# Kernel optimization log

Measured on AMD Instinct MI355X. Metric: run time of the kernel, lower is better.

The kernel has to match this reference:

```python
import jax, jax.numpy as jnp
import numpy as np

EPS = 1e-8

def _matrix_sqrt(cov):
    # e @ diag(max(w,EPS))**0.5 @ e.T
    w, e = jnp.linalg.eigh(cov)
    w = jnp.maximum(w, EPS)
    return (e * jnp.sqrt(w)[None, :]) @ e.T

def _matrix_sqrt_neg(cov):
    # cov jittered on diagonal, then e @ diag(1/max(w,EPS))**0.5 @ e.T
    D = cov.shape[-1]
    cov = cov * (jnp.ones_like(cov) + jnp.eye(D, dtype=cov.dtype) * 0.001)
    w, e = jnp.linalg.eigh(cov)
    w = jnp.maximum(w, EPS)
    return (e * (1.0 / jnp.sqrt(w))[None, :]) @ e.T

def _match_axis(xc, R, mu, counter):
    # xc: (C, M, D) per-channel rows; R: (C, D, D) accumulated second moment; mu: (C, D)
    mu_test = xc.mean(1, keepdims=True)                      # (C,1,D)
    h = xc - mu_test                                         # centered test features
    cov_train = R / counter - mu[:, :, None] * mu[:, None, :]  # (C,D,D)
    sqrt_train = jax.vmap(_matrix_sqrt)(cov_train)           # (C,D,D)
    M = h.shape[1]
    cov_test = jnp.einsum('cmd,cme->cde', h, h) / M          # (C,D,D)
    neg_sqrt_test = jax.vmap(_matrix_sqrt_neg)(cov_test)     # (C,D,D)
    T = jnp.einsum('cde,cef->cdf', neg_sqrt_test, sqrt_train)  # whiten-then-recolor map
    return jnp.einsum('cmd,cdf->cmf', h, T) + mu[:, None, :]

def reference(x, cov_H, mu_H, cov_W, mu_W, counter):
    N, H, W, C = x.shape
    cnt = jnp.asarray(counter, dtype=x.dtype)
    # H-axis matching: rows of length H, per channel
    xh = x.transpose(3, 0, 2, 1).reshape(C, N * W, H)
    xh = _match_axis(xh, cov_H, mu_H, cnt)
    # W-axis matching: rows of length W, per channel
    xw = xh.reshape(C, N, W, H).transpose(0, 1, 3, 2).reshape(C, N * H, W)
    xw = _match_axis(xw, cov_W, mu_W, cnt)
    return xw.reshape(C, N, H, W).transpose(1, 2, 3, 0)

def setup_inputs() -> dict:
    key = jax.random.key(0)
    k1, k2, k3, k4, k5 = jax.random.split(key, 5)
    N, H, W, C = 64, 56, 56, 256
    counter = 716800  # accumulated sample count (N*W per acc batch)
    x = jax.random.normal(k1, (N, H, W, C), dtype=jnp.float32)
    mu_H = 0.1 * jax.random.normal(k2, (C, H), dtype=jnp.float32)
    mu_W = 0.1 * jax.random.normal(k3, (C, W), dtype=jnp.float32)
    # Build accumulated second moments so R/counter - outer(mu) is PSD
    BH = jax.random.normal(k4, (C, H, H), dtype=jnp.float32)
    SH = jnp.einsum('cij,ckj->cik', BH, BH) / H + 0.1 * jnp.eye(H, dtype=jnp.float32)
    cov_H = (SH + mu_H[:, :, None] * mu_H[:, None, :]) * counter
    BW = jax.random.normal(k5, (C, W, W), dtype=jnp.float32)
    SW = jnp.einsum('cij,ckj->cik', BW, BW) / W + 0.1 * jnp.eye(W, dtype=jnp.float32)
    cov_W = (SW + mu_W[:, :, None] * mu_W[:, None, :]) * counter
    return {"x": x, "cov_H": cov_H, "mu_H": mu_H, "cov_W": cov_W, "mu_W": mu_W, "counter": counter}
```

## Files before the change

kernel.cpp:

```cpp
#include <hip/hip_runtime.h>

#define C_ 256
#define D_ 56
#define N_ 64
#define M_ 3584
#define DD_ 3136
#define PL_ 200704
#define PL4_ 50176
#define NS_ITERS 16

typedef __attribute__((ext_vector_type(8))) short v8s;
typedef __attribute__((ext_vector_type(8))) _Float16 v8h;
typedef __attribute__((ext_vector_type(4))) _Float16 v4h;
typedef __attribute__((ext_vector_type(4))) float v4f;

__device__ __forceinline__ unsigned short f2bf(float f) {
  union { float f; unsigned u; } x; x.f = f;
  unsigned r = x.u + 0x7FFFu + ((x.u >> 16) & 1u);
  return (unsigned short)(r >> 16);
}
__device__ __forceinline__ float bf2f(unsigned short h) {
  union { unsigned u; float f; } x; x.u = ((unsigned)h) << 16;
  return x.f;
}

__global__ __launch_bounds__(256) void k_tin(const float* __restrict__ x, float* __restrict__ A) {
  int b = blockIdx.x;
  int cchunk = b & 3, g = b >> 2;
  int c0 = cchunk * 64;
  int m0 = g * 4;
  int n = m0 / 56, w0 = m0 % 56;
  __shared__ float t[4][56][65];
  int tid = threadIdx.x;
  const float4* x4 = (const float4*)x;
  #pragma unroll
  for (int it = 0; it < 14; ++it) {
    int i = tid + 256*it;
    int mloc = i / 896, r = i % 896;
    int h = r >> 4, cg = r & 15;
    float4 v = x4[((size_t)n*3136 + (size_t)h*56 + (w0+mloc))*64 + (c0>>2) + cg];
    *(float4*)&t[mloc][h][4*cg] = v;
  }
  __syncthreads();
  float4* A4 = (float4*)A;
  #pragma unroll
  for (int it = 0; it < 14; ++it) {
    int j = tid + 256*it;
    int q = j / 14, hg = j % 14;
    int cc = q >> 2, mloc = q & 3;
    float4 o;
    o.x = t[mloc][4*hg+0][cc];
    o.y = t[mloc][4*hg+1][cc];
    o.z = t[mloc][4*hg+2][cc];
    o.w = t[mloc][4*hg+3][cc];
    A4[(size_t)(c0+cc)*PL4_ + (size_t)(m0+mloc)*14 + hg] = o;
  }
}

__device__ __forceinline__ void mm_split_h(const _Float16 (*Ah)[72], const _Float16 (*Al)[72],
                                           const _Float16 (*Bh)[72], const _Float16 (*Bl)[72],
                                           int w, int lr, int lq, v4f (&acc)[4]) {
  v8h ah[2], al[2], bh[4][2], bl[4][2];
  #pragma unroll
  for (int s = 0; s < 2; ++s) {
    int kb = 32*s + 8*lq;
    ah[s] = *(const v8h*)&Ah[16*w + lr][kb];
    al[s] = *(const v8h*)&Al[16*w + lr][kb];
    #pragma unroll
    for (int jt = 0; jt < 4; ++jt) {
      bh[jt][s] = *(const v8h*)&Bh[16*jt + lr][kb];
      bl[jt][s] = *(const v8h*)&Bl[16*jt + lr][kb];
    }
  }
  #pragma unroll
  for (int jt = 0; jt < 4; ++jt) {
    #pragma unroll
    for (int s = 0; s < 2; ++s) {
      acc[jt] = __builtin_amdgcn_mfma_f32_16x16x32_f16(ah[s], bh[jt][s], acc[jt], 0, 0, 0);
      acc[jt] = __builtin_amdgcn_mfma_f32_16x16x32_f16(ah[s], bl[jt][s], acc[jt], 0, 0, 0);
      acc[jt] = __builtin_amdgcn_mfma_f32_16x16x32_f16(al[s], bh[jt][s], acc[jt], 0, 0, 0);
    }
  }
}

__device__ __forceinline__ void store_split_h(_Float16 (*H)[72], _Float16 (*L)[72],
                                              int w, int lr, int lq, const v4f (&val)[4]) {
  #pragma unroll
  for (int jt = 0; jt < 4; ++jt) {
    #pragma unroll
    for (int e = 0; e < 4; ++e) {
      int i = 16*w + 4*lq + e, j = 16*jt + lr;
      float v = val[jt][e];
      _Float16 h = (_Float16)v;
      H[i][j] = h;
      L[i][j] = (_Float16)(v - (float)h);
    }
  }
}

__global__ __launch_bounds__(256) void k_stats(const float* __restrict__ in,
                                               float* __restrict__ muPart,
                                               float* __restrict__ covPart) {
  int b = blockIdx.x;
  int c = b >> 3, s = b & 7;
  const float* p = in + (size_t)c*PL_ + (size_t)(s*448)*56;
  __shared__ __align__(16) char lds[18432];
  unsigned short (*At)[72]  = (unsigned short(*)[72])lds;
  unsigned short (*Alt)[72] = (unsigned short(*)[72])(lds + 9216);
  float (*Qbuf)[66] = (float(*)[66])lds;
  float (*red2)[60] = (float(*)[60])lds;
  int tid = threadIdx.x;
  int cg = tid % 14, rg = tid / 14;
  bool act = tid < 224;
  float4 colsum = make_float4(0.f, 0.f, 0.f, 0.f);

  int l = tid & 63, w = tid >> 6;
  int lr = l & 15, lq = l >> 4;
  v4f zero4 = {0.f, 0.f, 0.f, 0.f};
  v4f accP[4], accQ[4];
  #pragma unroll
  for (int j = 0; j < 4; ++j) { accP[j] = zero4; accQ[j] = zero4; }

  for (int ch = 0; ch < 7; ++ch) {
    __syncthreads();
    const float4* p4 = (const float4*)(p + ch*64*56);
    if (act) {
      int c4 = cg * 4;
      #pragma unroll
      for (int u = 0; u < 4; ++u) {
        int m = u*16 + rg;
        float4 v = p4[m*14 + cg];
        colsum.x += v.x; colsum.y += v.y; colsum.z += v.z; colsum.w += v.w;
        unsigned short h;
        h = f2bf(v.x); At[c4+0][m] = h; Alt[c4+0][m] = f2bf(v.x - bf2f(h));
        h = f2bf(v.y); At[c4+1][m] = h; Alt[c4+1][m] = f2bf(v.y - bf2f(h));
        h = f2bf(v.z); At[c4+2][m] = h; Alt[c4+2][m] = f2bf(v.z - bf2f(h));
        h = f2bf(v.w); At[c4+3][m] = h; Alt[c4+3][m] = f2bf(v.w - bf2f(h));
      }
    }
    __syncthreads();
    #pragma unroll
    for (int s2 = 0; s2 < 2; ++s2) {
      int kb = 32*s2 + 8*lq;
      v8s a = *(const v8s*)&At[16*w + lr][kb];
      #pragma unroll
      for (int j = 0; j < 4; ++j) {
        v8s bh = *(const v8s*)&At[16*j + lr][kb];
        v8s bl = *(const v8s*)&Alt[16*j + lr][kb];
        accP[j] = __builtin_amdgcn_mfma_f32_16x16x32_bf16(a, bh, accP[j], 0, 0, 0);
        accQ[j] = __builtin_amdgcn_mfma_f32_16x16x32_bf16(a, bl, accQ[j], 0, 0, 0);
      }
    }
  }

  __syncthreads();
  if (act) *(float4*)&red2[rg][cg*4] = colsum;
  __syncthreads();
  if (tid < 64) {
    float m = 0.f;
    if (tid < 56) {
      #pragma unroll
      for (int r = 0; r < 16; ++r) m += red2[r][tid];
    }
    muPart[((size_t)s*C_ + c)*64 + tid] = m;
  }
  __syncthreads();

  #pragma unroll
  for (int j = 0; j < 4; ++j) {
    #pragma unroll
    for (int e = 0; e < 4; ++e) {
      int r = 16*w + 4*lq + e, cc = 16*j + lr;
      Qbuf[r][cc] = accQ[j][e];
    }
  }
  __syncthreads();
  float* op = covPart + ((size_t)s*C_ + c)*DD_;
  #pragma unroll
  for (int j = 0; j < 4; ++j) {
    #pragma unroll
    for (int e = 0; e < 4; ++e) {
      int r = 16*w + 4*lq + e, cc = 16*j + lr;
      if (r < 56 && cc < 56) op[r*56 + cc] = accP[j][e] + accQ[j][e] + Qbuf[cc][r];
    }
  }
}

__global__ __launch_bounds__(256) void k_mured(const float* __restrict__ muPart, float* __restrict__ muT) {
  int idx = blockIdx.x*256 + threadIdx.x;
  if (idx >= C_*64) return;
  int c = idx >> 6, lane = idx & 63;
  float s = 0.f;
  for (int p = 0; p < 8; ++p) s += muPart[((size_t)p*C_ + c)*64 + lane];
  muT[idx] = s * (1.0f/M_);
}

__global__ __launch_bounds__(256) void k_finalize(const float* __restrict__ covPart, const float* __restrict__ muT,
                                                  const float* __restrict__ covIn, const float* __restrict__ muTrn,
                                                  const int* __restrict__ counter,
                                                  float* __restrict__ covTest, float* __restrict__ covTr) {
  int idx = blockIdx.x*256 + threadIdx.x;
  const int total = C_*DD_;
  if (idx < total) {
    int c = idx / DD_, r2 = idx % DD_, i = r2/56, j = r2%56;
    float ssum = 0.f;
    for (int s = 0; s < 8; ++s) ssum += covPart[((size_t)s*C_ + c)*DD_ + r2];
    float v = ssum*(1.0f/M_) - muT[c*64+i]*muT[c*64+j];
    if (i == j) v *= 1.001f;
    covTest[idx] = v;
  } else if (idx < 2*total) {
    int k = idx - total;
    int c = k / DD_, r2 = k % DD_, i = r2/56, j = r2%56;
    float cnt = (float)counter[0];
    covTr[k] = covIn[k]/cnt - muTrn[c*56+i]*muTrn[c*56+j];
  }
}

__global__ __launch_bounds__(256) void k_ns(const float* __restrict__ covTr, const float* __restrict__ covTest,
                                            float* __restrict__ Sout, float* __restrict__ Zout) {
  __shared__ __align__(16) _Float16 mats[6][64][72];
  __shared__ float red[4];
  int tid = threadIdx.x;
  int which = blockIdx.x & 1, c = blockIdx.x >> 1;
  const float4* Ain4 = (const float4*)((which ? covTest : covTr) + (size_t)c * DD_);

  typedef _Float16 (*mat_t)[72];
  mat_t Yh = mats[0], Yl = mats[1], Zh = mats[2], Zl = mats[3], Th = mats[4], Tl = mats[5];

  float ss = 0.f;
  for (int i4 = tid; i4 < 784; i4 += 256) {
    float4 v = Ain4[i4];
    ss += v.x*v.x + v.y*v.y + v.z*v.z + v.w*v.w;
  }
  { unsigned* z = (unsigned*)mats; for (int i = tid; i < 13824; i += 256) z[i] = 0u; }
  #pragma unroll
  for (int off = 32; off > 0; off >>= 1) ss += __shfl_down(ss, off, 64);
  if ((tid & 63) == 0) red[tid >> 6] = ss;
  __syncthreads();
  float s = sqrtf(red[0] + red[1] + red[2] + red[3]);
  float inv = 1.f / s;

  for (int i4 = tid; i4 < 784; i4 += 256) {
    float4 v = Ain4[i4];
    int r = i4 / 14, cgx = (i4 % 14) * 4;
    float f0 = v.x*inv, f1 = v.y*inv, f2 = v.z*inv, f3 = v.w*inv;
    v4h hh, ll;
    hh.x = (_Float16)f0; ll.x = (_Float16)(f0 - (float)hh.x);
    hh.y = (_Float16)f1; ll.y = (_Float16)(f1 - (float)hh.y);
    hh.z = (_Float16)f2; ll.z = (_Float16)(f2 - (float)hh.z);
    hh.w = (_Float16)f3; ll.w = (_Float16)(f3 - (float)hh.w);
    *(v4h*)&Yh[r][cgx] = hh;
    *(v4h*)&Yl[r][cgx] = ll;
  }
  if (tid < 56) Zh[tid][tid] = (_Float16)1.0f;
  __syncthreads();

  int lane = tid & 63, w = tid >> 6, lr = lane & 15, lq = lane >> 4;
  v4f zero4 = {0.f, 0.f, 0.f, 0.f};
  float rs = sqrtf(s);
  float fac = which ? (1.f/rs) : rs;
  float* outp = (which ? Zout : Sout) + (size_t)c*DD_;

  for (int it = 0; it < NS_ITERS; ++it) {
    v4f accW[4] = {zero4, zero4, zero4, zero4};
    mm_split_h(Zh, Zl, Yh, Yl, w, lr, lq, accW);
    v4f Tv[4];
    #pragma unroll
    for (int jt = 0; jt < 4; ++jt) {
      #pragma unroll
      for (int e = 0; e < 4; ++e) {
        float dv = (16*w + 4*lq + e == 16*jt + lr) ? 1.5f : 0.f;
        Tv[jt][e] = dv - 0.5f*accW[jt][e];
      }
    }
    store_split_h(Th, Tl, w, lr, lq, Tv);
    __syncthreads();
    if (it == NS_ITERS - 1) {
      v4f accF[4] = {zero4, zero4, zero4, zero4};
      if (which == 0) mm_split_h(Yh, Yl, Th, Tl, w, lr, lq, accF);
      else            mm_split_h(Th, Tl, Zh, Zl, w, lr, lq, accF);
      #pragma unroll
      for (int jt = 0; jt < 4; ++jt) {
        #pragma unroll
        for (int e = 0; e < 4; ++e) {
          int i = 16*w + 4*lq + e, j = 16*jt + lr;
          if (i < 56 && j < 56) outp[i*56 + j] = accF[jt][e] * fac;
        }
      }
    } else {
      v4f accY[4] = {zero4, zero4, zero4, zero4};
      v4f accZ[4] = {zero4, zero4, zero4, zero4};
      mm_split_h(Yh, Yl, Th, Tl, w, lr, lq, accY);
      mm_split_h(Th, Tl, Zh, Zl, w, lr, lq, accZ);
      __syncthreads();
      store_split_h(Yh, Yl, w, lr, lq, accY);
      store_split_h(Zh, Zl, w, lr, lq, accZ);
      __syncthreads();
    }
  }
}

__global__ __launch_bounds__(256) void k_tmap(const float* __restrict__ Zi, const float* __restrict__ Sm,
                                              float* __restrict__ Tm) {
  __shared__ __align__(16) _Float16 mats[4][64][72];
  int c = blockIdx.x, tid = threadIdx.x;
  typedef _Float16 (*mat_t)[72];
  mat_t Ah = mats[0], Al = mats[1], Bh = mats[2], Bl = mats[3];
  { unsigned* z = (unsigned*)mats; for (int i = tid; i < 9216; i += 256) z[i] = 0u; }
  __syncthreads();
  const float4* Z4 = (const float4*)(Zi + (size_t)c*DD_);
  const float4* S4 = (const float4*)(Sm + (size_t)c*DD_);
  for (int i4 = tid; i4 < 784; i4 += 256) {
    int r = i4 / 14, cgx = (i4 % 14) * 4;
    float4 v = Z4[i4];
    v4h hh, ll;
    hh.x = (_Float16)v.x; ll.x = (_Float16)(v.x - (float)hh.x);
    hh.y = (_Float16)v.y; ll.y = (_Float16)(v.y - (float)hh.y);
    hh.z = (_Float16)v.z; ll.z = (_Float16)(v.z - (float)hh.z);
    hh.w = (_Float16)v.w; ll.w = (_Float16)(v.w - (float)hh.w);
    *(v4h*)&Ah[r][cgx] = hh;
    *(v4h*)&Al[r][cgx] = ll;
    v = S4[i4];
    hh.x = (_Float16)v.x; ll.x = (_Float16)(v.x - (float)hh.x);
    hh.y = (_Float16)v.y; ll.y = (_Float16)(v.y - (float)hh.y);
    hh.z = (_Float16)v.z; ll.z = (_Float16)(v.z - (float)hh.z);
    hh.w = (_Float16)v.w; ll.w = (_Float16)(v.w - (float)hh.w);
    *(v4h*)&Bh[r][cgx] = hh;
    *(v4h*)&Bl[r][cgx] = ll;
  }
  __syncthreads();
  int lane = tid & 63, w = tid >> 6, lr = lane & 15, lq = lane >> 4;
  v4f zero4 = {0.f, 0.f, 0.f, 0.f};
  v4f acc[4] = {zero4, zero4, zero4, zero4};
  mm_split_h(Ah, Al, Bh, Bl, w, lr, lq, acc);
  float* op = Tm + (size_t)c*DD_;
  #pragma unroll
  for (int jt = 0; jt < 4; ++jt) {
    #pragma unroll
    for (int e = 0; e < 4; ++e) {
      int i = 16*w + 4*lq + e, j = 16*jt + lr;
      if (i < 56 && j < 56) op[i*56 + j] = acc[jt][e];
    }
  }
}

__global__ __launch_bounds__(256) void k_apply(const float* __restrict__ in, const float* __restrict__ muT,
                                               const float* __restrict__ Tmp, const float* __restrict__ muTrain,
                                               float* __restrict__ out, int stage) {
  int b = blockIdx.x;
  int c = b >> 6, n = b & 63;
  __shared__ __align__(16) char lds[18432];
  _Float16 (*Abf)[72] = (_Float16(*)[72])lds;
  _Float16 (*Tt)[72]  = (_Float16(*)[72])(lds + 9216);
  float (*Y)[67] = (float(*)[67])lds;
  __shared__ float smu[64], smt[64];
  int tid = threadIdx.x;
  if (tid < 64) {
    smu[tid] = muT[c*64 + tid];
    smt[tid] = (tid < 56) ? muTrain[c*56 + tid] : 0.f;
  }
  if (tid < 128) {
    int row = tid & 63;
    _Float16 (*Mz)[72] = (tid < 64) ? Abf : Tt;
    *(float4*)&Mz[row][56] = make_float4(0.f, 0.f, 0.f, 0.f);
  }
  __syncthreads();
  const float4* p4 = (const float4*)(in + (size_t)c*PL_ + (size_t)n*3136);
  const float4* t4 = (const float4*)(Tmp + (size_t)c*DD_);
  for (int i = tid; i < 784; i += 256) {
    float4 v = p4[i];
    int row = i / 14, cgx = (i % 14) * 4;
    v4h pk;
    pk.x = (_Float16)(v.x - smu[cgx+0]);
    pk.y = (_Float16)(v.y - smu[cgx+1]);
    pk.z = (_Float16)(v.z - smu[cgx+2]);
    pk.w = (_Float16)(v.w - smu[cgx+3]);
    *(v4h*)&Abf[row][cgx] = pk;
    float4 t = t4[i];
    Tt[cgx+0][row] = (_Float16)t.x;
    Tt[cgx+1][row] = (_Float16)t.y;
    Tt[cgx+2][row] = (_Float16)t.z;
    Tt[cgx+3][row] = (_Float16)t.w;
  }
  __syncthreads();
  int l = tid & 63, w = tid >> 6;
  int lr = l & 15, lq = l >> 4;
  v4f zero4 = {0.f, 0.f, 0.f, 0.f};
  v4f acc[4];
  #pragma unroll
  for (int j = 0; j < 4; ++j) acc[j] = zero4;
  #pragma unroll
  for (int s = 0; s < 2; ++s) {
    int kb = 32*s + 8*lq;
    v8h a = *(const v8h*)&Abf[16*w + lr][kb];
    #pragma unroll
    for (int j = 0; j < 4; ++j) {
      v8h bb = *(const v8h*)&Tt[16*j + lr][kb];
      acc[j] = __builtin_amdgcn_mfma_f32_16x16x32_f16(a, bb, acc[j], 0, 0, 0);
    }
  }
  __syncthreads();
  #pragma unroll
  for (int j = 0; j < 4; ++j) {
    #pragma unroll
    for (int e = 0; e < 4; ++e) {
      int r = 16*w + 4*lq + e, cc = 16*j + lr;
      Y[r][cc] = acc[j][e] + smt[cc];
    }
  }
  __syncthreads();
  float4* op4 = (float4*)(out + (size_t)c*PL_ + (size_t)n*3136);
  if (stage == 1) {
    for (int i4 = tid; i4 < 784; i4 += 256) {
      int h = i4 / 14, w4 = (i4 % 14) * 4;
      float4 o;
      o.x = Y[w4+0][h]; o.y = Y[w4+1][h]; o.z = Y[w4+2][h]; o.w = Y[w4+3][h];
      op4[i4] = o;
    }
  } else {
    for (int i4 = tid; i4 < 784; i4 += 256) {
      int h = i4 / 14, w4 = (i4 % 14) * 4;
      float4 o;
      o.x = Y[h][w4+0]; o.y = Y[h][w4+1]; o.z = Y[h][w4+2]; o.w = Y[h][w4+3];
      op4[i4] = o;
    }
  }
}

__global__ __launch_bounds__(256) void k_tout(const float* __restrict__ A2, float* __restrict__ out) {
  int b = blockIdx.x;
  int cchunk = b & 3, g = b >> 2;
  int c0 = cchunk * 64;
  int nh0 = g * 4;
  __shared__ float t[4][56][65];
  int tid = threadIdx.x;
  const float4* A4 = (const float4*)A2;
  #pragma unroll
  for (int it = 0; it < 14; ++it) {
    int j = tid + 256*it;
    int q = j / 14, wg = j % 14;
    int cc = q >> 2, mloc = q & 3;
    float4 v = A4[(size_t)(c0+cc)*PL4_ + (size_t)(nh0+mloc)*14 + wg];
    t[mloc][4*wg+0][cc] = v.x;
    t[mloc][4*wg+1][cc] = v.y;
    t[mloc][4*wg+2][cc] = v.z;
    t[mloc][4*wg+3][cc] = v.w;
  }
  __syncthreads();
  float4* o4 = (float4*)out;
  #pragma unroll
  for (int it = 0; it < 14; ++it) {
    int i = tid + 256*it;
    int mloc = i / 896, r = i % 896;
    int w = r >> 4, cg = r & 15;
    float4 o;
    o.x = t[mloc][w][4*cg+0];
    o.y = t[mloc][w][4*cg+1];
    o.z = t[mloc][w][4*cg+2];
    o.w = t[mloc][w][4*cg+3];
    o4[((size_t)(nh0+mloc)*56 + w)*64 + (c0>>2) + cg] = o;
  }
}

extern "C" void kernel_launch(void* const* d_in, const int* in_sizes, int n_in,
                              void* d_out, int out_size, void* d_ws, size_t ws_size,
                              hipStream_t stream) {
  (void)in_sizes; (void)n_in; (void)out_size;
  const float* x    = (const float*)d_in[0];
  const float* covH = (const float*)d_in[1];
  const float* muH  = (const float*)d_in[2];
  const float* covW = (const float*)d_in[3];
  const float* muW  = (const float*)d_in[4];
  const int*   cnt  = (const int*)d_in[5];
  float* out = (float*)d_out;

  char* ws = (char*)d_ws;
  size_t off = 0;
  auto alloc = [&](size_t nfloats) {
    float* p = (float*)(ws + off);
    off += ((nfloats*sizeof(float) + 255) / 256) * 256;
    return p;
  };
  float* A       = alloc((size_t)C_ * PL_);
  float* covPart = alloc((size_t)8 * C_ * DD_);
  float* muPart  = alloc((size_t)8 * C_ * 64);
  float* covTest = alloc((size_t)C_ * DD_);
  float* covTr   = alloc((size_t)C_ * DD_);
  float* Sm      = alloc((size_t)C_ * DD_);
  float* Zim     = alloc((size_t)C_ * DD_);
  float* Tm      = alloc((size_t)C_ * DD_);
  float* muT     = alloc((size_t)C_ * 64);
  if (off > ws_size) return;

  dim3 blk(256);
  const int finGrid = (2*C_*DD_ + 255)/256;

  k_tin<<<dim3(4 * (M_/4)), blk, 0, stream>>>(x, A);

  k_stats   <<<dim3(2048),  blk, 0, stream>>>(A, muPart, covPart);
  k_mured   <<<dim3(64),    blk, 0, stream>>>(muPart, muT);
  k_finalize<<<dim3(finGrid), blk, 0, stream>>>(covPart, muT, covH, muH, cnt, covTest, covTr);
  k_ns      <<<dim3(512),   blk, 0, stream>>>(covTr, covTest, Sm, Zim);
  k_tmap    <<<dim3(256),   blk, 0, stream>>>(Zim, Sm, Tm);
  k_apply   <<<dim3(16384), blk, 0, stream>>>(A, muT, Tm, muH, out, 1);

  k_stats   <<<dim3(2048),  blk, 0, stream>>>(out, muPart, covPart);
  k_mured   <<<dim3(64),    blk, 0, stream>>>(muPart, muT);
  k_finalize<<<dim3(finGrid), blk, 0, stream>>>(covPart, muT, covW, muW, cnt, covTest, covTr);
  k_ns      <<<dim3(512),   blk, 0, stream>>>(covTr, covTest, Sm, Zim);
  k_tmap    <<<dim3(256),   blk, 0, stream>>>(Zim, Sm, Tm);
  k_apply   <<<dim3(16384), blk, 0, stream>>>(out, muT, Tm, muW, A, 2);

  k_tout<<<dim3(4 * (M_/4)), blk, 0, stream>>>(A, out);
}
```

Measured before the change: 579.5 us.

## Store intermediate activation planes in fp16 instead of fp32

The channel-major intermediate buffers written by the input transpose and by each apply stage, and read by the stats, apply and output transpose kernels, become half precision instead of fp32. This halves the global memory traffic of these bandwidth-bound passes, and the load/store loops are rewritten around 8-wide fp16 vectors. The cost is precision: inputs are rounded to fp16 before the covariance statistics are computed. The bf16 hi/lo split used in the statistics therefore no longer recovers full fp32 accuracy, which may loosen agreement with the fp32 reference.

Measured after the change: 500.0 us. 1.16x faster.

```diff
diff --git a/kernel.cpp b/kernel.cpp
--- a/kernel.cpp
+++ b/kernel.cpp
@@ -6,7 +6,6 @@
 #define M_ 3584
 #define DD_ 3136
 #define PL_ 200704
-#define PL4_ 50176
 #define NS_ITERS 16
 
 typedef __attribute__((ext_vector_type(8))) short v8s;
@@ -24,13 +23,13 @@
   return x.f;
 }
 
-__global__ __launch_bounds__(256) void k_tin(const float* __restrict__ x, float* __restrict__ A) {
+__global__ __launch_bounds__(256) void k_tin(const float* __restrict__ x, _Float16* __restrict__ A) {
   int b = blockIdx.x;
   int cchunk = b & 3, g = b >> 2;
   int c0 = cchunk * 64;
   int m0 = g * 4;
   int n = m0 / 56, w0 = m0 % 56;
-  __shared__ float t[4][56][65];
+  __shared__ _Float16 t[4][56][66];
   int tid = threadIdx.x;
   const float4* x4 = (const float4*)x;
   #pragma unroll
@@ -39,21 +38,21 @@
     int mloc = i / 896, r = i % 896;
     int h = r >> 4, cg = r & 15;
     float4 v = x4[((size_t)n*3136 + (size_t)h*56 + (w0+mloc))*64 + (c0>>2) + cg];
-    *(float4*)&t[mloc][h][4*cg] = v;
-  }
-  __syncthreads();
-  float4* A4 = (float4*)A;
-  #pragma unroll
-  for (int it = 0; it < 14; ++it) {
+    t[mloc][h][4*cg+0] = (_Float16)v.x;
+    t[mloc][h][4*cg+1] = (_Float16)v.y;
+    t[mloc][h][4*cg+2] = (_Float16)v.z;
+    t[mloc][h][4*cg+3] = (_Float16)v.w;
+  }
+  __syncthreads();
+  #pragma unroll
+  for (int it = 0; it < 7; ++it) {
     int j = tid + 256*it;
-    int q = j / 14, hg = j % 14;
+    int q = j / 7, hg = j % 7;
     int cc = q >> 2, mloc = q & 3;
-    float4 o;
-    o.x = t[mloc][4*hg+0][cc];
-    o.y = t[mloc][4*hg+1][cc];
-    o.z = t[mloc][4*hg+2][cc];
-    o.w = t[mloc][4*hg+3][cc];
-    A4[(size_t)(c0+cc)*PL4_ + (size_t)(m0+mloc)*14 + hg] = o;
+    v8h o;
+    #pragma unroll
+    for (int k = 0; k < 8; ++k) o[k] = t[mloc][hg*8+k][cc];
+    *(v8h*)&A[(size_t)(c0+cc)*PL_ + (size_t)(m0+mloc)*56 + hg*8] = o;
   }
 }
 
@@ -98,21 +97,21 @@
   }
 }
 
-__global__ __launch_bounds__(256) void k_stats(const float* __restrict__ in,
+__global__ __launch_bounds__(256) void k_stats(const _Float16* __restrict__ in,
                                                float* __restrict__ muPart,
                                                float* __restrict__ covPart) {
   int b = blockIdx.x;
   int c = b >> 3, s = b & 7;
-  const float* p = in + (size_t)c*PL_ + (size_t)(s*448)*56;
+  const _Float16* p = in + (size_t)c*PL_ + (size_t)(s*448)*56;
   __shared__ __align__(16) char lds[18432];
   unsigned short (*At)[72]  = (unsigned short(*)[72])lds;
   unsigned short (*Alt)[72] = (unsigned short(*)[72])(lds + 9216);
   float (*Qbuf)[66] = (float(*)[66])lds;
   float (*red2)[60] = (float(*)[60])lds;
   int tid = threadIdx.x;
-  int cg = tid % 14, rg = tid / 14;
+  int cg = tid % 7, rg = tid / 7;
   bool act = tid < 224;
-  float4 colsum = make_float4(0.f, 0.f, 0.f, 0.f);
+  float cs[8] = {0.f,0.f,0.f,0.f,0.f,0.f,0.f,0.f};
 
   int l = tid & 63, w = tid >> 6;
   int lr = l & 15, lq = l >> 4;
@@ -123,19 +122,19 @@
 
   for (int ch = 0; ch < 7; ++ch) {
     __syncthreads();
-    const float4* p4 = (const float4*)(p + ch*64*56);
     if (act) {
-      int c4 = cg * 4;
-      #pragma unroll
-      for (int u = 0; u < 4; ++u) {
-        int m = u*16 + rg;
-        float4 v = p4[m*14 + cg];
-        colsum.x += v.x; colsum.y += v.y; colsum.z += v.z; colsum.w += v.w;
-        unsigned short h;
-        h = f2bf(v.x); At[c4+0][m] = h; Alt[c4+0][m] = f2bf(v.x - bf2f(h));
-        h = f2bf(v.y); At[c4+1][m] = h; Alt[c4+1][m] = f2bf(v.y - bf2f(h));
-        h = f2bf(v.z); At[c4+2][m] = h; Alt[c4+2][m] = f2bf(v.z - bf2f(h));
-        h = f2bf(v.w); At[c4+3][m] = h; Alt[c4+3][m] = f2bf(v.w - bf2f(h));
+      #pragma unroll
+      for (int u = 0; u < 2; ++u) {
+        int m = rg + 32*u;
+        v8h v = *(const v8h*)&p[(size_t)(ch*64 + m)*56 + cg*8];
+        #pragma unroll
+        for (int k = 0; k < 8; ++k) {
+          float f = (float)v[k];
+          cs[k] += f;
+          unsigned short h = f2bf(f);
+          At[cg*8+k][m] = h;
+          Alt[cg*8+k][m] = f2bf(f - bf2f(h));
+        }
       }
     }
     __syncthreads();
@@ -154,13 +153,16 @@
   }
 
   __syncthreads();
-  if (act) *(float4*)&red2[rg][cg*4] = colsum;
+  if (act) {
+    #pragma unroll
+    for (int k = 0; k < 8; ++k) red2[rg][cg*8+k] = cs[k];
+  }
   __syncthreads();
   if (tid < 64) {
     float m = 0.f;
     if (tid < 56) {
       #pragma unroll
-      for (int r = 0; r < 16; ++r) m += red2[r][tid];
+      for (int r = 0; r < 32; ++r) m += red2[r][tid];
     }
     muPart[((size_t)s*C_ + c)*64 + tid] = m;
   }
@@ -344,9 +346,9 @@
   }
 }
 
-__global__ __launch_bounds__(256) void k_apply(const float* __restrict__ in, const float* __restrict__ muT,
+__global__ __launch_bounds__(256) void k_apply(const _Float16* __restrict__ in, const float* __restrict__ muT,
                                                const float* __restrict__ Tmp, const float* __restrict__ muTrain,
-                                               float* __restrict__ out, int stage) {
+                                               _Float16* __restrict__ out, int stage) {
   int b = blockIdx.x;
   int c = b >> 6, n = b & 63;
   __shared__ __align__(16) char lds[18432];
@@ -365,18 +367,19 @@
     *(float4*)&Mz[row][56] = make_float4(0.f, 0.f, 0.f, 0.f);
   }
   __syncthreads();
-  const float4* p4 = (const float4*)(in + (size_t)c*PL_ + (size_t)n*3136);
+  const v8h* p8 = (const v8h*)(in + (size_t)c*PL_ + (size_t)n*3136);
   const float4* t4 = (const float4*)(Tmp + (size_t)c*DD_);
+  for (int i = tid; i < 392; i += 256) {
+    int row = i / 7, cg = i % 7;
+    v8h v = p8[row*7 + cg];
+    v8h pk;
+    #pragma unroll
+    for (int k = 0; k < 8; ++k) pk[k] = (_Float16)((float)v[k] - smu[cg*8+k]);
+    *(v8h*)&Abf[row][cg*8] = pk;
+  }
   for (int i = tid; i < 784; i += 256) {
-    float4 v = p4[i];
+    float4 t = t4[i];
     int row = i / 14, cgx = (i % 14) * 4;
-    v4h pk;
-    pk.x = (_Float16)(v.x - smu[cgx+0]);
-    pk.y = (_Float16)(v.y - smu[cgx+1]);
-    pk.z = (_Float16)(v.z - smu[cgx+2]);
-    pk.w = (_Float16)(v.w - smu[cgx+3]);
-    *(v4h*)&Abf[row][cgx] = pk;
-    float4 t = t4[i];
     Tt[cgx+0][row] = (_Float16)t.x;
     Tt[cgx+1][row] = (_Float16)t.y;
     Tt[cgx+2][row] = (_Float16)t.z;
@@ -409,42 +412,41 @@
     }
   }
   __syncthreads();
-  float4* op4 = (float4*)(out + (size_t)c*PL_ + (size_t)n*3136);
+  _Float16* o16 = out + (size_t)c*PL_ + (size_t)n*3136;
   if (stage == 1) {
-    for (int i4 = tid; i4 < 784; i4 += 256) {
-      int h = i4 / 14, w4 = (i4 % 14) * 4;
-      float4 o;
-      o.x = Y[w4+0][h]; o.y = Y[w4+1][h]; o.z = Y[w4+2][h]; o.w = Y[w4+3][h];
-      op4[i4] = o;
+    for (int i = tid; i < 392; i += 256) {
+      int h = i / 7, wg = i % 7;
+      v8h o;
+      #pragma unroll
+      for (int k = 0; k < 8; ++k) o[k] = (_Float16)Y[wg*8+k][h];
+      *(v8h*)&o16[h*56 + wg*8] = o;
     }
   } else {
-    for (int i4 = tid; i4 < 784; i4 += 256) {
-      int h = i4 / 14, w4 = (i4 % 14) * 4;
-      float4 o;
-      o.x = Y[h][w4+0]; o.y = Y[h][w4+1]; o.z = Y[h][w4+2]; o.w = Y[h][w4+3];
-      op4[i4] = o;
-    }
-  }
-}
-
-__global__ __launch_bounds__(256) void k_tout(const float* __restrict__ A2, float* __restrict__ out) {
+    for (int i = tid; i < 392; i += 256) {
+      int h = i / 7, wg = i % 7;
+      v8h o;
+      #pragma unroll
+      for (int k = 0; k < 8; ++k) o[k] = (_Float16)Y[h][wg*8+k];
+      *(v8h*)&o16[h*56 + wg*8] = o;
+    }
+  }
+}
+
+__global__ __launch_bounds__(256) void k_tout(const _Float16* __restrict__ A2, float* __restrict__ out) {
   int b = blockIdx.x;
   int cchunk = b & 3, g = b >> 2;
   int c0 = cchunk * 64;
   int nh0 = g * 4;
-  __shared__ float t[4][56][65];
+  __shared__ _Float16 t[4][56][66];
   int tid = threadIdx.x;
-  const float4* A4 = (const float4*)A2;
-  #pragma unroll
-  for (int it = 0; it < 14; ++it) {
+  #pragma unroll
+  for (int it = 0; it < 7; ++it) {
     int j = tid + 256*it;
-    int q = j / 14, wg = j % 14;
+    int q = j / 7, wg = j % 7;
     int cc = q >> 2, mloc = q & 3;
-    float4 v = A4[(size_t)(c0+cc)*PL4_ + (size_t)(nh0+mloc)*14 + wg];
-    t[mloc][4*wg+0][cc] = v.x;
-    t[mloc][4*wg+1][cc] = v.y;
-    t[mloc][4*wg+2][cc] = v.z;
-    t[mloc][4*wg+3][cc] = v.w;
+    v8h v = *(const v8h*)&A2[(size_t)(c0+cc)*PL_ + (size_t)(nh0+mloc)*56 + wg*8];
+    #pragma unroll
+    for (int k = 0; k < 8; ++k) t[mloc][wg*8+k][cc] = v[k];
   }
   __syncthreads();
   float4* o4 = (float4*)out;
@@ -454,10 +456,10 @@
     int mloc = i / 896, r = i % 896;
     int w = r >> 4, cg = r & 15;
     float4 o;
-    o.x = t[mloc][w][4*cg+0];
-    o.y = t[mloc][w][4*cg+1];
-    o.z = t[mloc][w][4*cg+2];
-    o.w = t[mloc][w][4*cg+3];
+    o.x = (float)t[mloc][w][4*cg+0];
+    o.y = (float)t[mloc][w][4*cg+1];
+    o.z = (float)t[mloc][w][4*cg+2];
+    o.w = (float)t[mloc][w][4*cg+3];
     o4[((size_t)(nh0+mloc)*56 + w)*64 + (c0>>2) + cg] = o;
   }
 }
@@ -476,40 +478,41 @@
 
   char* ws = (char*)d_ws;
   size_t off = 0;
-  auto alloc = [&](size_t nfloats) {
-    float* p = (float*)(ws + off);
-    off += ((nfloats*sizeof(float) + 255) / 256) * 256;
+  auto allocB = [&](size_t nbytes) {
+    void* p = ws + off;
+    off += ((nbytes + 255) / 256) * 256;
     return p;
   };
-  float* A       = alloc((size_t)C_ * PL_);
-  float* covPart = alloc((size_t)8 * C_ * DD_);
-  float* muPart  = alloc((size_t)8 * C_ * 64);
-  float* covTest = alloc((size_t)C_ * DD_);
-  float* covTr   = alloc((size_t)C_ * DD_);
-  float* Sm      = alloc((size_t)C_ * DD_);
-  float* Zim     = alloc((size_t)C_ * DD_);
-  float* Tm      = alloc((size_t)C_ * DD_);
-  float* muT     = alloc((size_t)C_ * 64);
+  _Float16* A16a  = (_Float16*)allocB((size_t)C_ * PL_ * 2);
+  _Float16* A16b  = (_Float16*)allocB((size_t)C_ * PL_ * 2);
+  float* covPart  = (float*)allocB((size_t)8 * C_ * DD_ * 4);
+  float* muPart   = (float*)allocB((size_t)8 * C_ * 64 * 4);
+  float* covTest  = (float*)allocB((size_t)C_ * DD_ * 4);
+  float* covTr    = (float*)allocB((size_t)C_ * DD_ * 4);
+  float* Sm       = (float*)allocB((size_t)C_ * DD_ * 4);
+  float* Zim      = (float*)allocB((size_t)C_ * DD_ * 4);
+  float* Tm       = (float*)allocB((size_t)C_ * DD_ * 4);
+  float* muT      = (float*)allocB((size_t)C_ * 64 * 4);
   if (off > ws_size) return;
 
   dim3 blk(256);
   const int finGrid = (2*C_*DD_ + 255)/256;
 
-  k_tin<<<dim3(4 * (M_/4)), blk, 0, stream>>>(x, A);
-
-  k_stats   <<<dim3(2048),  blk, 0, stream>>>(A, muPart, covPart);
+  k_tin<<<dim3(4 * (M_/4)), blk, 0, stream>>>(x, A16a);
+
+  k_stats   <<<dim3(2048),  blk, 0, stream>>>(A16a, muPart, covPart);
   k_mured   <<<dim3(64),    blk, 0, stream>>>(muPart, muT);
   k_finalize<<<dim3(finGrid), blk, 0, stream>>>(covPart, muT, covH, muH, cnt, covTest, covTr);
   k_ns      <<<dim3(512),   blk, 0, stream>>>(covTr, covTest, Sm, Zim);
   k_tmap    <<<dim3(256),   blk, 0, stream>>>(Zim, Sm, Tm);
-  k_apply   <<<dim3(16384), blk, 0, stream>>>(A, muT, Tm, muH, out, 1);
-
-  k_stats   <<<dim3(2048),  blk, 0, stream>>>(out, muPart, covPart);
+  k_apply   <<<dim3(16384), blk, 0, stream>>>(A16a, muT, Tm, muH, A16b, 1);
+
+  k_stats   <<<dim3(2048),  blk, 0, stream>>>(A16b, muPart, covPart);
   k_mured   <<<dim3(64),    blk, 0, stream>>>(muPart, muT);
   k_finalize<<<dim3(finGrid), blk, 0, stream>>>(covPart, muT, covW, muW, cnt, covTest, covTr);
   k_ns      <<<dim3(512),   blk, 0, stream>>>(covTr, covTest, Sm, Zim);
   k_tmap    <<<dim3(256),   blk, 0, stream>>>(Zim, Sm, Tm);
-  k_apply   <<<dim3(16384), blk, 0, stream>>>(out, muT, Tm, muW, A, 2);
-
-  k_tout<<<dim3(4 * (M_/4)), blk, 0, stream>>>(A, out);
-}
+  k_apply   <<<dim3(16384), blk, 0, stream>>>(A16b, muT, Tm, muW, A16a, 2);
+
+  k_tout<<<dim3(4 * (M_/4)), blk, 0, stream>>>(A16a, out);
+}
```
